# Kernel tuning notes

Measured on AMD Instinct MI355X. Metric: run time of the kernel, lower is better.

Reference implementation:

```python
import jax, jax.numpy as jnp
import numpy as np

FEATURES = 4096
BATCH = 2048


def setup_inputs() -> dict:
    key = jax.random.key(0)
    kx, kk = jax.random.split(key)
    x = jax.random.normal(kx, (BATCH, FEATURES), dtype=jnp.float32)
    kernel = jax.random.normal(kk, (FEATURES,), dtype=jnp.float32)
    return {"x": x, "kernel": kernel}


def reference(x, kernel):
    n = kernel.shape[0]
    i = jnp.arange(n)[:, None]   # [n,1]
    j = jnp.arange(n)[None, :]   # [1,n]
    idx = i - j                   # Toeplitz offsets
    # W[i,j] = kernel[i-j] if i>=j else 0  (causal lower-triangular Toeplitz)
    W = jnp.where(idx >= 0, kernel[jnp.clip(idx, 0, n - 1)], 0.0)
    # out[b,i] = sum_{j<=i} x[b,j] * kernel[i-j]  == x @ W.T
    return x @ W.T
```

## Files before the change

### kernel.cpp

```cpp
#include <hip/hip_runtime.h>
#include <hip/hip_bf16.h>


typedef unsigned short u16;
typedef __attribute__((ext_vector_type(8))) short  bf16x8;
typedef __attribute__((ext_vector_type(8))) unsigned short u16x8;
typedef __attribute__((ext_vector_type(4))) float  f32x4;

#define KDIM 4096
#define NDIM 4096
#define MDIM 2048
#define KREV_STRIDE 4608
#define KREV_BYTES  (8 * KREV_STRIDE * 2)

#define MFMA_BF16 __builtin_amdgcn_mfma_f32_16x16x32_bf16

static __device__ inline u16 f2bf(float f) {
  unsigned u = __builtin_bit_cast(unsigned, f);
  unsigned r = u + 0x7FFFu + ((u >> 16) & 1u);
  return (u16)(r >> 16);
}

static __device__ inline void async_copy16(const void* g, void* l) {
  __builtin_amdgcn_global_load_lds((const __attribute__((address_space(1))) void*)g,
                                   (__attribute__((address_space(3))) void*)l,
                                   16, 0, 0);
}

__global__ __launch_bounds__(256) void prep(const float* __restrict__ x,
                                            const float* __restrict__ kern,
                                            u16* __restrict__ xb,
                                            u16* __restrict__ krevs,
                                            int conv_blocks) {
  int kblk = (int)blockIdx.x - conv_blocks;
  if (kblk >= 0) {
    int u = kblk * 256 + threadIdx.x;
    for (int a = 0; a < 8; ++a) {
      int t = u + a - 8;
      u16 v = 0;
      if (t >= 0 && t <= 4095) v = f2bf(kern[4095 - t]);
      krevs[a * KREV_STRIDE + u] = v;
    }
  } else {
    unsigned tg  = blockIdx.x * 256 + threadIdx.x;
    unsigned l   = tg & 63;
    unsigned kb  = (tg >> 6) & 127;
    unsigned rg  = tg >> 13;
    unsigned row = rg * 16 + (l & 15);
    unsigned k   = kb * 32 + (l >> 4) * 8;
    const f32x4* p = (const f32x4*)(x + (size_t)row * KDIM + k);
    f32x4 v0 = p[0], v1 = p[1];
    u16x8 r;
    r[0] = f2bf(v0[0]); r[1] = f2bf(v0[1]); r[2] = f2bf(v0[2]); r[3] = f2bf(v0[3]);
    r[4] = f2bf(v1[0]); r[5] = f2bf(v1[1]); r[6] = f2bf(v1[2]); r[7] = f2bf(v1[3]);
    *(u16x8*)(xb + (size_t)tg * 8) = r;
  }
}

template <bool CONV>
__global__ __launch_bounds__(512, 4) void toeplitz_gemm(const void* __restrict__ Av,
                                                        const u16* __restrict__ krevs,
                                                        float* __restrict__ out) {
  __shared__ __align__(16) char smem_raw[68736];
  u16*   B_all = (u16*)smem_raw;
  f32x4* ep    = (f32x4*)smem_raw;

  const int tid  = threadIdx.x;
  const int w    = tid >> 6;
  const int g    = w >> 2;
  const int wl   = w & 3;
  const int lane = tid & 63;
  const int lane16 = lane & 15;
  const int quad   = lane >> 4;
  const int wm = wl >> 1;
  const int wn = wl & 1;

  const int b  = (int)blockIdx.x;
  const int x_ = b & 7;
  const int jj = b >> 3;
  const int q  = jj & 31;
  const int h2 = jj >> 5;
  const int mt = x_ + 8 * (q & 1);
  const int ct = h2 ? (q >> 1) : 31 - (q >> 1);
  const int n0 = ct * 128;
  const int m0 = mt * 128;
  const int W  = 3968 - n0;

  const int LEN_e    = 128 * (ct + 1) + 160;
  const int stride_e = 128 * (ct + 1) + 200;

  int boff[4];
  for (int fn = 0; fn < 4; ++fn) {
    int n_g = n0 + wn * 64 + fn * 16 + lane16;
    int s0  = 4095 - n_g + quad * 8;
    int a   = s0 & 7;
    boff[fn] = a * stride_e + (s0 - a + 8 - W);
  }

  f32x4 acc[4][4] = {};

  const int wmu = __builtin_amdgcn_readfirstlane(wm);
  const int gu  = __builtin_amdgcn_readfirstlane(g);
  const u16*   xb2 = (const u16*)Av;
  const float* xf  = (const float*)Av;
  int aoffs[4];
  for (int fm = 0; fm < 4; ++fm)
    aoffs[fm] = (mt * 8 + wmu * 4 + fm) * 65536 + gu * 1024 + lane * 8;
  const int rowb = m0 + wm * 64 + lane16;

  auto ldA = [&](int fm, int t, int kk) -> bf16x8 {
    return *(const bf16x8*)(xb2 + aoffs[fm] + t * 2048 + kk * 512);
  };
  auto ldAc = [&](int fm, int t, int kk) -> bf16x8 {
    const float* px = xf + (size_t)(rowb + fm * 16) * KDIM +
                      t * 128 + gu * 64 + kk * 32 + quad * 8;
    f32x4 v0 = *(const f32x4*)px, v1 = *(const f32x4*)(px + 4);
    u16x8 r;
    r[0]=f2bf(v0[0]); r[1]=f2bf(v0[1]); r[2]=f2bf(v0[2]); r[3]=f2bf(v0[3]);
    r[4]=f2bf(v1[0]); r[5]=f2bf(v1[1]); r[6]=f2bf(v1[2]); r[7]=f2bf(v1[3]);
    return __builtin_bit_cast(bf16x8, r);
  };

  {
    const u16* src = krevs + w * KREV_STRIDE + W;
    char* dstb = smem_raw + (size_t)w * stride_e * 2;
    for (int c = 0; c * 512 < LEN_e; ++c) {
      int idx = c * 512 + lane * 8;
      if (idx < LEN_e)
        async_copy16(src + idx, dstb + (size_t)c * 1024);
    }
  }
  asm volatile("s_waitcnt vmcnt(0)" ::: "memory");
  __builtin_amdgcn_s_barrier();
  asm volatile("" ::: "memory");

  if constexpr (!CONV) {
    bf16x8 afA[4], afB[4];
#pragma unroll
    for (int fm = 0; fm < 4; ++fm) afA[fm] = ldA(fm, 0, 0);
#pragma unroll
    for (int fm = 0; fm < 4; ++fm) afB[fm] = ldA(fm, 0, 1);
    for (int t = 0; ; ++t) {
      const int ks = t * 128 + g * 64;
#pragma unroll
      for (int fn = 0; fn < 4; ++fn) {
        bf16x8 bv = *(const bf16x8*)(&B_all[boff[fn] + ks]);
#pragma unroll
        for (int fm = 0; fm < 4; ++fm)
          acc[fm][fn] = MFMA_BF16(afA[fm], bv, acc[fm][fn], 0, 0, 0);
      }
      if (t < ct)
#pragma unroll
        for (int fm = 0; fm < 4; ++fm) afA[fm] = ldA(fm, t + 1, 0);
#pragma unroll
      for (int fn = 0; fn < 4; ++fn) {
        bf16x8 bv = *(const bf16x8*)(&B_all[boff[fn] + ks + 32]);
#pragma unroll
        for (int fm = 0; fm < 4; ++fm)
          acc[fm][fn] = MFMA_BF16(afB[fm], bv, acc[fm][fn], 0, 0, 0);
      }
      if (t == ct) break;
#pragma unroll
      for (int fm = 0; fm < 4; ++fm) afB[fm] = ldA(fm, t + 1, 1);
    }
  } else {
    for (int t = 0; t <= ct; ++t) {
      const int ks = t * 128 + g * 64;
#pragma unroll
      for (int kk = 0; kk < 2; ++kk) {
        bf16x8 af[4];
#pragma unroll
        for (int fm = 0; fm < 4; ++fm) af[fm] = ldAc(fm, t, kk);
#pragma unroll
        for (int fn = 0; fn < 4; ++fn) {
          bf16x8 bv = *(const bf16x8*)(&B_all[boff[fn] + ks + kk * 32]);
#pragma unroll
          for (int fm = 0; fm < 4; ++fm)
            acc[fm][fn] = MFMA_BF16(af[fm], bv, acc[fm][fn], 0, 0, 0);
        }
      }
    }
  }

  const int j = tid & 255;
  for (int r = 0; r < 2; ++r) {
    __syncthreads();
    if (g == 1) {
      for (int fm2 = 0; fm2 < 2; ++fm2)
        for (int fn = 0; fn < 4; ++fn)
          ep[j * 9 + fm2 * 4 + fn] = acc[r * 2 + fm2][fn];
    }
    __syncthreads();
    if (g == 0) {
      for (int fm2 = 0; fm2 < 2; ++fm2)
        for (int fn = 0; fn < 4; ++fn)
          acc[r * 2 + fm2][fn] += ep[j * 9 + fm2 * 4 + fn];
    }
  }

  if (g == 0) {
    for (int fm = 0; fm < 4; ++fm) {
      int row_base = m0 + wm * 64 + fm * 16 + quad * 4;
      for (int fn = 0; fn < 4; ++fn) {
        int col = n0 + wn * 64 + fn * 16 + lane16;
        for (int r = 0; r < 4; ++r)
          out[(size_t)(row_base + r) * NDIM + col] = acc[fm][fn][r];
      }
    }
  }
}

extern "C" void kernel_launch(void* const* d_in, const int* in_sizes, int n_in,
                              void* d_out, int out_size, void* d_ws, size_t ws_size,
                              hipStream_t stream) {
  const float* x    = (const float*)d_in[0];
  const float* kern = (const float*)d_in[1];
  float* out = (float*)d_out;

  u16* krevs = (u16*)d_ws;
  u16* xb    = (u16*)((char*)d_ws + KREV_BYTES);
  const size_t need_fast = (size_t)KREV_BYTES + (size_t)MDIM * KDIM * 2;

  if (ws_size >= need_fast) {
    prep<<<4096 + 18, 256, 0, stream>>>(x, kern, xb, krevs, 4096);
    toeplitz_gemm<false><<<512, 512, 0, stream>>>(xb, krevs, out);
  } else {
    prep<<<18, 256, 0, stream>>>(x, kern, xb, krevs, 0);
    toeplitz_gemm<true><<<512, 512, 0, stream>>>(x, krevs, out);
  }
}
```

Baseline: 117.0 us.

## Pair complementary triangular column tiles per block with half-height row tiles

Each block now covers 64 rows instead of 128 and processes two column tiles, ct and 31-ct, one after the other. Because the triangle gives column tile ct a K extent of ct+1 steps, this pairing hands every block the same amount of work and removes the imbalance between blocks. Both kernel windows are staged into shared memory up front, and each phase does its own split-K reduction and store. In exchange, each B fragment read from shared memory now feeds two MFMAs instead of four, and LDS use per block grows.

```diff
diff --git a/kernel.cpp b/kernel.cpp
--- a/kernel.cpp
+++ b/kernel.cpp
@@ -61,7 +61,7 @@
 __global__ __launch_bounds__(512, 4) void toeplitz_gemm(const void* __restrict__ Av,
                                                         const u16* __restrict__ krevs,
                                                         float* __restrict__ out) {
-  __shared__ __align__(16) char smem_raw[68736];
+  __shared__ __align__(16) char smem_raw[73984];
   u16*   B_all = (u16*)smem_raw;
   f32x4* ep    = (f32x4*)smem_raw;
 
@@ -75,38 +75,30 @@
   const int wm = wl >> 1;
   const int wn = wl & 1;
 
-  const int b  = (int)blockIdx.x;
-  const int x_ = b & 7;
-  const int jj = b >> 3;
-  const int q  = jj & 31;
-  const int h2 = jj >> 5;
-  const int mt = x_ + 8 * (q & 1);
-  const int ct = h2 ? (q >> 1) : 31 - (q >> 1);
-  const int n0 = ct * 128;
-  const int m0 = mt * 128;
-  const int W  = 3968 - n0;
-
-  const int LEN_e    = 128 * (ct + 1) + 160;
-  const int stride_e = 128 * (ct + 1) + 200;
-
-  int boff[4];
-  for (int fn = 0; fn < 4; ++fn) {
-    int n_g = n0 + wn * 64 + fn * 16 + lane16;
-    int s0  = 4095 - n_g + quad * 8;
-    int a   = s0 & 7;
-    boff[fn] = a * stride_e + (s0 - a + 8 - W);
-  }
-
-  f32x4 acc[4][4] = {};
+  const int b   = (int)blockIdx.x;
+  const int x_  = b & 7;
+  const int jj  = b >> 3;
+  const int p_  = x_ + 8 * (jj & 1);
+  const int mt2 = p_ * 2 + ((jj >> 1) & 1);
+  const int ctp = jj >> 2;
+  const int ct1 = 31 - ctp;
+  const int ct2 = ctp;
+  const int m0  = mt2 * 64;
+
+  const int len1 = 128 * (ct1 + 1) + 160, stride1 = len1 + 40;
+  const int len2 = 128 * (ct2 + 1) + 160, stride2 = len2 + 40;
+  const int base2 = 8 * stride1;
+  const int W1 = 3968 - 128 * ct1;
+  const int W2 = 3968 - 128 * ct2;
 
   const int wmu = __builtin_amdgcn_readfirstlane(wm);
   const int gu  = __builtin_amdgcn_readfirstlane(g);
   const u16*   xb2 = (const u16*)Av;
   const float* xf  = (const float*)Av;
-  int aoffs[4];
-  for (int fm = 0; fm < 4; ++fm)
-    aoffs[fm] = (mt * 8 + wmu * 4 + fm) * 65536 + gu * 1024 + lane * 8;
-  const int rowb = m0 + wm * 64 + lane16;
+  int aoffs[2];
+  for (int fm = 0; fm < 2; ++fm)
+    aoffs[fm] = (mt2 * 4 + wmu * 2 + fm) * 65536 + gu * 1024 + lane * 8;
+  const int rowb = m0 + wm * 32 + lane16;
 
   auto ldA = [&](int fm, int t, int kk) -> bf16x8 {
     return *(const bf16x8*)(xb2 + aoffs[fm] + t * 2048 + kk * 512);
@@ -121,93 +113,104 @@
     return __builtin_bit_cast(bf16x8, r);
   };
 
-  {
-    const u16* src = krevs + w * KREV_STRIDE + W;
-    char* dstb = smem_raw + (size_t)w * stride_e * 2;
-    for (int c = 0; c * 512 < LEN_e; ++c) {
+  auto stageWin = [&](int base_e, int stride_e, int len_e, int Wp) {
+    const u16* src = krevs + w * KREV_STRIDE + Wp;
+    char* dstb = smem_raw + (size_t)(base_e + w * stride_e) * 2;
+    for (int c = 0; c * 512 < len_e; ++c) {
       int idx = c * 512 + lane * 8;
-      if (idx < LEN_e)
+      if (idx < len_e)
         async_copy16(src + idx, dstb + (size_t)c * 1024);
     }
-  }
+  };
+  stageWin(0, stride1, len1, W1);
+  stageWin(base2, stride2, len2, W2);
   asm volatile("s_waitcnt vmcnt(0)" ::: "memory");
   __builtin_amdgcn_s_barrier();
   asm volatile("" ::: "memory");
 
-  if constexpr (!CONV) {
-    bf16x8 afA[4], afB[4];
-#pragma unroll
-    for (int fm = 0; fm < 4; ++fm) afA[fm] = ldA(fm, 0, 0);
-#pragma unroll
-    for (int fm = 0; fm < 4; ++fm) afB[fm] = ldA(fm, 0, 1);
-    for (int t = 0; ; ++t) {
-      const int ks = t * 128 + g * 64;
-#pragma unroll
-      for (int fn = 0; fn < 4; ++fn) {
-        bf16x8 bv = *(const bf16x8*)(&B_all[boff[fn] + ks]);
-#pragma unroll
-        for (int fm = 0; fm < 4; ++fm)
-          acc[fm][fn] = MFMA_BF16(afA[fm], bv, acc[fm][fn], 0, 0, 0);
+  auto runPhase = [&](int ctq, int base_e, int stride_q, int Wq) {
+    const int n0q = ctq * 128;
+    int boff[4];
+    for (int fn = 0; fn < 4; ++fn) {
+      int n_g = n0q + wn * 64 + fn * 16 + lane16;
+      int s0  = 4095 - n_g + quad * 8;
+      int a   = s0 & 7;
+      boff[fn] = base_e + a * stride_q + (s0 - a + 8 - Wq);
+    }
+    f32x4 acc[2][4] = {};
+
+    if constexpr (!CONV) {
+      bf16x8 afA[2], afB[2];
+#pragma unroll
+      for (int fm = 0; fm < 2; ++fm) afA[fm] = ldA(fm, 0, 0);
+#pragma unroll
+      for (int fm = 0; fm < 2; ++fm) afB[fm] = ldA(fm, 0, 1);
+      for (int t = 0; ; ++t) {
+        const int ks = t * 128 + g * 64;
+#pragma unroll
+        for (int fn = 0; fn < 4; ++fn) {
+          bf16x8 bv = *(const bf16x8*)(&B_all[boff[fn] + ks]);
+#pragma unroll
+          for (int fm = 0; fm < 2; ++fm)
+            acc[fm][fn] = MFMA_BF16(afA[fm], bv, acc[fm][fn], 0, 0, 0);
+        }
+        if (t < ctq)
+#pragma unroll
+          for (int fm = 0; fm < 2; ++fm) afA[fm] = ldA(fm, t + 1, 0);
+#pragma unroll
+        for (int fn = 0; fn < 4; ++fn) {
+          bf16x8 bv = *(const bf16x8*)(&B_all[boff[fn] + ks + 32]);
+#pragma unroll
+          for (int fm = 0; fm < 2; ++fm)
+            acc[fm][fn] = MFMA_BF16(afB[fm], bv, acc[fm][fn], 0, 0, 0);
+        }
+        if (t == ctq) break;
+#pragma unroll
+        for (int fm = 0; fm < 2; ++fm) afB[fm] = ldA(fm, t + 1, 1);
       }
-      if (t < ct)
-#pragma unroll
-        for (int fm = 0; fm < 4; ++fm) afA[fm] = ldA(fm, t + 1, 0);
-#pragma unroll
-      for (int fn = 0; fn < 4; ++fn) {
-        bf16x8 bv = *(const bf16x8*)(&B_all[boff[fn] + ks + 32]);
-#pragma unroll
-        for (int fm = 0; fm < 4; ++fm)
-          acc[fm][fn] = MFMA_BF16(afB[fm], bv, acc[fm][fn], 0, 0, 0);
+    } else {
+      for (int t = 0; t <= ctq; ++t) {
+        const int ks = t * 128 + g * 64;
+#pragma unroll
+        for (int kk = 0; kk < 2; ++kk) {
+          bf16x8 af[2];
+#pragma unroll
+          for (int fm = 0; fm < 2; ++fm) af[fm] = ldAc(fm, t, kk);
+#pragma unroll
+          for (int fn = 0; fn < 4; ++fn) {
+            bf16x8 bv = *(const bf16x8*)(&B_all[boff[fn] + ks + kk * 32]);
+#pragma unroll
+            for (int fm = 0; fm < 2; ++fm)
+              acc[fm][fn] = MFMA_BF16(af[fm], bv, acc[fm][fn], 0, 0, 0);
+          }
+        }
       }
-      if (t == ct) break;
-#pragma unroll
-      for (int fm = 0; fm < 4; ++fm) afB[fm] = ldA(fm, t + 1, 1);
-    }
-  } else {
-    for (int t = 0; t <= ct; ++t) {
-      const int ks = t * 128 + g * 64;
-#pragma unroll
-      for (int kk = 0; kk < 2; ++kk) {
-        bf16x8 af[4];
-#pragma unroll
-        for (int fm = 0; fm < 4; ++fm) af[fm] = ldAc(fm, t, kk);
-#pragma unroll
-        for (int fn = 0; fn < 4; ++fn) {
-          bf16x8 bv = *(const bf16x8*)(&B_all[boff[fn] + ks + kk * 32]);
-#pragma unroll
-          for (int fm = 0; fm < 4; ++fm)
-            acc[fm][fn] = MFMA_BF16(af[fm], bv, acc[fm][fn], 0, 0, 0);
-        }
-      }
-    }
-  }
-
-  const int j = tid & 255;
-  for (int r = 0; r < 2; ++r) {
+    }
+
+    const int j = tid & 255;
     __syncthreads();
     if (g == 1) {
-      for (int fm2 = 0; fm2 < 2; ++fm2)
+      for (int fm = 0; fm < 2; ++fm)
         for (int fn = 0; fn < 4; ++fn)
-          ep[j * 9 + fm2 * 4 + fn] = acc[r * 2 + fm2][fn];
+          ep[j * 9 + fm * 4 + fn] = acc[fm][fn];
     }
     __syncthreads();
     if (g == 0) {
-      for (int fm2 = 0; fm2 < 2; ++fm2)
-        for (int fn = 0; fn < 4; ++fn)
-          acc[r * 2 + fm2][fn] += ep[j * 9 + fm2 * 4 + fn];
-    }
-  }
-
-  if (g == 0) {
-    for (int fm = 0; fm < 4; ++fm) {
-      int row_base = m0 + wm * 64 + fm * 16 + quad * 4;
-      for (int fn = 0; fn < 4; ++fn) {
-        int col = n0 + wn * 64 + fn * 16 + lane16;
-        for (int r = 0; r < 4; ++r)
-          out[(size_t)(row_base + r) * NDIM + col] = acc[fm][fn][r];
-      }
-    }
-  }
+      for (int fm = 0; fm < 2; ++fm)
+        for (int fn = 0; fn < 4; ++fn) {
+          f32x4 v = acc[fm][fn];
+          f32x4 o = ep[j * 9 + fm * 4 + fn];
+          v[0] += o[0]; v[1] += o[1]; v[2] += o[2]; v[3] += o[3];
+          int row_base = m0 + wm * 32 + fm * 16 + quad * 4;
+          int col = n0q + wn * 64 + fn * 16 + lane16;
+          for (int r = 0; r < 4; ++r)
+            out[(size_t)(row_base + r) * NDIM + col] = v[r];
+        }
+    }
+  };
+
+  runPhase(ct1, 0, stride1, W1);
+  runPhase(ct2, base2, stride2, W2);
 }
 
 extern "C" void kernel_launch(void* const* d_in, const int* in_sizes, int n_in,
```

Measured after the change: 112.8 us. 3.6% less time.

## Pair complementary triangular column tiles per block for balanced work

Applied to the files above, without the earlier changes.

Each block now handles two 64-wide column strips from complementary column tiles (ct and 31-ct), so every block does about the same number of K steps instead of work varying with the tile's position in the triangle. Both Toeplitz kernel windows are staged into LDS up front, and each phase uses a 4x2 MFMA fragment tile with its own reduction and store. This removes load imbalance and tail effects across the grid. In exchange it uses slightly more LDS, runs two sequential phases with extra barriers, and halves the N-reuse of each A fragment load.

```diff
diff --git a/kernel.cpp b/kernel.cpp
--- a/kernel.cpp
+++ b/kernel.cpp
@@ -61,7 +61,7 @@
 __global__ __launch_bounds__(512, 4) void toeplitz_gemm(const void* __restrict__ Av,
                                                         const u16* __restrict__ krevs,
                                                         float* __restrict__ out) {
-  __shared__ __align__(16) char smem_raw[68736];
+  __shared__ __align__(16) char smem_raw[69888];
   u16*   B_all = (u16*)smem_raw;
   f32x4* ep    = (f32x4*)smem_raw;
 
@@ -75,29 +75,21 @@
   const int wm = wl >> 1;
   const int wn = wl & 1;
 
-  const int b  = (int)blockIdx.x;
-  const int x_ = b & 7;
-  const int jj = b >> 3;
-  const int q  = jj & 31;
-  const int h2 = jj >> 5;
-  const int mt = x_ + 8 * (q & 1);
-  const int ct = h2 ? (q >> 1) : 31 - (q >> 1);
-  const int n0 = ct * 128;
-  const int m0 = mt * 128;
-  const int W  = 3968 - n0;
-
-  const int LEN_e    = 128 * (ct + 1) + 160;
-  const int stride_e = 128 * (ct + 1) + 200;
-
-  int boff[4];
-  for (int fn = 0; fn < 4; ++fn) {
-    int n_g = n0 + wn * 64 + fn * 16 + lane16;
-    int s0  = 4095 - n_g + quad * 8;
-    int a   = s0 & 7;
-    boff[fn] = a * stride_e + (s0 - a + 8 - W);
-  }
-
-  f32x4 acc[4][4] = {};
+  const int b   = (int)blockIdx.x;
+  const int x_  = b & 7;
+  const int jj  = b >> 3;
+  const int p_  = x_ + 8 * (jj & 1);
+  const int ctp = (jj >> 1) & 15;
+  const int cn  = jj >> 5;
+  const int ct1 = 31 - ctp;
+  const int ct2 = ctp;
+  const int m0  = p_ * 128;
+
+  const int stride1 = 128 * (ct1 + 1) + 72;
+  const int stride2 = 128 * (ct2 + 1) + 72;
+  const int base2   = 8 * stride1;
+  const int W1 = 4032 - (ct1 * 128 + cn * 64);
+  const int W2 = 4032 - (ct2 * 128 + cn * 64);
 
   const int wmu = __builtin_amdgcn_readfirstlane(wm);
   const int gu  = __builtin_amdgcn_readfirstlane(g);
@@ -105,7 +97,7 @@
   const float* xf  = (const float*)Av;
   int aoffs[4];
   for (int fm = 0; fm < 4; ++fm)
-    aoffs[fm] = (mt * 8 + wmu * 4 + fm) * 65536 + gu * 1024 + lane * 8;
+    aoffs[fm] = (p_ * 8 + wmu * 4 + fm) * 65536 + gu * 1024 + lane * 8;
   const int rowb = m0 + wm * 64 + lane16;
 
   auto ldA = [&](int fm, int t, int kk) -> bf16x8 {
@@ -121,93 +113,109 @@
     return __builtin_bit_cast(bf16x8, r);
   };
 
-  {
-    const u16* src = krevs + w * KREV_STRIDE + W;
-    char* dstb = smem_raw + (size_t)w * stride_e * 2;
-    for (int c = 0; c * 512 < LEN_e; ++c) {
+  auto stageWin = [&](int base_e, int stride_e, int Wp) {
+    const u16* src = krevs + w * KREV_STRIDE + Wp;
+    char* dstb = smem_raw + (size_t)(base_e + w * stride_e) * 2;
+    for (int c = 0; c * 512 < stride_e; ++c) {
       int idx = c * 512 + lane * 8;
-      if (idx < LEN_e)
+      if (idx < stride_e)
         async_copy16(src + idx, dstb + (size_t)c * 1024);
     }
-  }
+  };
+  stageWin(0, stride1, W1);
+  stageWin(base2, stride2, W2);
   asm volatile("s_waitcnt vmcnt(0)" ::: "memory");
   __builtin_amdgcn_s_barrier();
   asm volatile("" ::: "memory");
 
-  if constexpr (!CONV) {
-    bf16x8 afA[4], afB[4];
-#pragma unroll
-    for (int fm = 0; fm < 4; ++fm) afA[fm] = ldA(fm, 0, 0);
-#pragma unroll
-    for (int fm = 0; fm < 4; ++fm) afB[fm] = ldA(fm, 0, 1);
-    for (int t = 0; ; ++t) {
-      const int ks = t * 128 + g * 64;
-#pragma unroll
-      for (int fn = 0; fn < 4; ++fn) {
-        bf16x8 bv = *(const bf16x8*)(&B_all[boff[fn] + ks]);
-#pragma unroll
-        for (int fm = 0; fm < 4; ++fm)
-          acc[fm][fn] = MFMA_BF16(afA[fm], bv, acc[fm][fn], 0, 0, 0);
-      }
-      if (t < ct)
-#pragma unroll
-        for (int fm = 0; fm < 4; ++fm) afA[fm] = ldA(fm, t + 1, 0);
-#pragma unroll
-      for (int fn = 0; fn < 4; ++fn) {
-        bf16x8 bv = *(const bf16x8*)(&B_all[boff[fn] + ks + 32]);
-#pragma unroll
-        for (int fm = 0; fm < 4; ++fm)
-          acc[fm][fn] = MFMA_BF16(afB[fm], bv, acc[fm][fn], 0, 0, 0);
-      }
-      if (t == ct) break;
-#pragma unroll
-      for (int fm = 0; fm < 4; ++fm) afB[fm] = ldA(fm, t + 1, 1);
-    }
-  } else {
-    for (int t = 0; t <= ct; ++t) {
-      const int ks = t * 128 + g * 64;
-#pragma unroll
-      for (int kk = 0; kk < 2; ++kk) {
-        bf16x8 af[4];
-#pragma unroll
-        for (int fm = 0; fm < 4; ++fm) af[fm] = ldAc(fm, t, kk);
-#pragma unroll
-        for (int fn = 0; fn < 4; ++fn) {
-          bf16x8 bv = *(const bf16x8*)(&B_all[boff[fn] + ks + kk * 32]);
+  auto runPhase = [&](int ctq, int base_e, int stride_q, int Wq) {
+    const int n0c = ctq * 128 + cn * 64;
+    int boff[2];
+    for (int fn = 0; fn < 2; ++fn) {
+      int n_g = n0c + wn * 32 + fn * 16 + lane16;
+      int s0  = 4095 - n_g + quad * 8;
+      int a   = s0 & 7;
+      boff[fn] = base_e + a * stride_q + (s0 - a + 8 - Wq);
+    }
+    f32x4 acc[4][2] = {};
+
+    if constexpr (!CONV) {
+      bf16x8 afA[4], afB[4];
+#pragma unroll
+      for (int fm = 0; fm < 4; ++fm) afA[fm] = ldA(fm, 0, 0);
+#pragma unroll
+      for (int fm = 0; fm < 4; ++fm) afB[fm] = ldA(fm, 0, 1);
+      for (int t = 0; ; ++t) {
+        const int ks = t * 128 + g * 64;
+#pragma unroll
+        for (int fn = 0; fn < 2; ++fn) {
+          bf16x8 bv = *(const bf16x8*)(&B_all[boff[fn] + ks]);
 #pragma unroll
           for (int fm = 0; fm < 4; ++fm)
-            acc[fm][fn] = MFMA_BF16(af[fm], bv, acc[fm][fn], 0, 0, 0);
+            acc[fm][fn] = MFMA_BF16(afA[fm], bv, acc[fm][fn], 0, 0, 0);
         }
-      }
-    }
-  }
-
-  const int j = tid & 255;
-  for (int r = 0; r < 2; ++r) {
+        if (t < ctq)
+#pragma unroll
+          for (int fm = 0; fm < 4; ++fm) afA[fm] = ldA(fm, t + 1, 0);
+#pragma unroll
+        for (int fn = 0; fn < 2; ++fn) {
+          bf16x8 bv = *(const bf16x8*)(&B_all[boff[fn] + ks + 32]);
+#pragma unroll
+          for (int fm = 0; fm < 4; ++fm)
+            acc[fm][fn] = MFMA_BF16(afB[fm], bv, acc[fm][fn], 0, 0, 0);
+        }
+        if (t == ctq) break;
+#pragma unroll
+        for (int fm = 0; fm < 4; ++fm) afB[fm] = ldA(fm, t + 1, 1);
+      }
+    } else {
+      for (int t = 0; t <= ctq; ++t) {
+        const int ks = t * 128 + g * 64;
+#pragma unroll
+        for (int kk = 0; kk < 2; ++kk) {
+          bf16x8 af[4];
+#pragma unroll
+          for (int fm = 0; fm < 4; ++fm) af[fm] = ldAc(fm, t, kk);
+#pragma unroll
+          for (int fn = 0; fn < 2; ++fn) {
+            bf16x8 bv = *(const bf16x8*)(&B_all[boff[fn] + ks + kk * 32]);
+#pragma unroll
+            for (int fm = 0; fm < 4; ++fm)
+              acc[fm][fn] = MFMA_BF16(af[fm], bv, acc[fm][fn], 0, 0, 0);
+          }
+        }
+      }
+    }
+
+    const int j = tid & 255;
     __syncthreads();
-    if (g == 1) {
-      for (int fm2 = 0; fm2 < 2; ++fm2)
-        for (int fn = 0; fn < 4; ++fn)
-          ep[j * 9 + fm2 * 4 + fn] = acc[r * 2 + fm2][fn];
-    }
-    __syncthreads();
-    if (g == 0) {
-      for (int fm2 = 0; fm2 < 2; ++fm2)
-        for (int fn = 0; fn < 4; ++fn)
-          acc[r * 2 + fm2][fn] += ep[j * 9 + fm2 * 4 + fn];
-    }
-  }
-
-  if (g == 0) {
-    for (int fm = 0; fm < 4; ++fm) {
-      int row_base = m0 + wm * 64 + fm * 16 + quad * 4;
-      for (int fn = 0; fn < 4; ++fn) {
-        int col = n0 + wn * 64 + fn * 16 + lane16;
-        for (int r = 0; r < 4; ++r)
-          out[(size_t)(row_base + r) * NDIM + col] = acc[fm][fn][r];
-      }
-    }
-  }
+#pragma unroll
+    for (int r = 0; r < 2; ++r) {
+      if (r) __syncthreads();
+      if (g == 1) {
+        for (int fm2 = 0; fm2 < 2; ++fm2)
+          for (int fn = 0; fn < 2; ++fn)
+            ep[j * 5 + fm2 * 2 + fn] = acc[r * 2 + fm2][fn];
+      }
+      __syncthreads();
+      if (g == 0) {
+        for (int fm2 = 0; fm2 < 2; ++fm2)
+          for (int fn = 0; fn < 2; ++fn) {
+            f32x4 v = acc[r * 2 + fm2][fn];
+            f32x4 o = ep[j * 5 + fm2 * 2 + fn];
+            v[0] += o[0]; v[1] += o[1]; v[2] += o[2]; v[3] += o[3];
+            int fm = r * 2 + fm2;
+            int row_base = m0 + wm * 64 + fm * 16 + quad * 4;
+            int col = n0c + wn * 32 + fn * 16 + lane16;
+            for (int rr = 0; rr < 4; ++rr)
+              out[(size_t)(row_base + rr) * NDIM + col] = v[rr];
+          }
+      }
+    }
+  };
+
+  runPhase(ct1, 0, stride1, W1);
+  runPhase(ct2, base2, stride2, W2);
 }
 
 extern "C" void kernel_launch(void* const* d_in, const int* in_sizes, int n_in,
```

New measurement: 123.9 us. 5.9% more time.
